# Optimization experiments

Measured on AMD Instinct MI355X. Metric: run time of the kernel, lower is better.

Reference implementation:

```python
import jax, jax.numpy as jnp
import numpy as np

B, S, D = 4, 4096, 1024


def setup_inputs() -> dict:
    key = jax.random.key(0)
    ks = jax.random.split(key, 7)
    scale = 1.0 / np.sqrt(D)
    return {
        "x": jax.random.normal(ks[0], (B, S, D), dtype=jnp.float32),
        "W_in": jax.random.normal(ks[1], (D, D), dtype=jnp.float32) * scale,
        "W_select": jax.random.normal(ks[2], (D, D), dtype=jnp.float32) * scale,
        "W_gate": jax.random.normal(ks[3], (D, D), dtype=jnp.float32) * scale,
        "W_out": jax.random.normal(ks[4], (D, D), dtype=jnp.float32) * scale,
        "W_delta": jax.random.normal(ks[5], (D, D), dtype=jnp.float32) * scale,
        "log_a": jax.random.normal(ks[6], (D,), dtype=jnp.float32) * 0.1,
    }


def reference(x, W_in, W_select, W_gate, W_out, W_delta, log_a):
    # diag mode of ChaosSSMCore. nn.Linear(bias=False): y = x @ W.T
    a_base = jax.nn.sigmoid(log_a).astype(x.dtype)  # [D]
    # Precompute all per-step projections in batched GEMMs: [B,S,D]
    delta = jnp.maximum(jax.nn.softplus(jnp.einsum('bsd,ed->bse', x, W_delta)), 1e-4)
    decay = jnp.exp(-delta * a_base)                                   # [B,S,D]
    update = jax.nn.sigmoid(jnp.einsum('bsd,ed->bse', x, W_select)) \
        * jnp.tanh(jnp.einsum('bsd,ed->bse', x, W_in))                 # [B,S,D]
    gate = jax.nn.sigmoid(jnp.einsum('bsd,ed->bse', x, W_gate))        # [B,S,D]

    def step(state, inputs):
        dec_t, upd_t = inputs
        state = dec_t * state + upd_t
        return state, state

    init = jnp.zeros((x.shape[0], x.shape[2]), dtype=x.dtype)
    # scan over seq axis: move to [S,B,D]
    _, states = jax.lax.scan(step, init, (decay.transpose(1, 0, 2), update.transpose(1, 0, 2)))
    states = states.transpose(1, 0, 2)  # [B,S,D]
    out = gate * states
    y = jnp.einsum('bsd,ed->bse', out, W_out)
    return y
```

## Files before the change

### kernel.cpp

```cpp
#include <hip/hip_runtime.h>
#include <hip/hip_bf16.h>
#include <math.h>

#define B_   4
#define S_   4096
#define D_   1024
#define M_   (B_*S_)
#define NCAT (4*D_)
#define KD   1024

#define NCHUNK 128
#define CHLEN  (S_/NCHUNK)

typedef __bf16 bf16x8 __attribute__((ext_vector_type(8)));
typedef float  f32x4  __attribute__((ext_vector_type(4)));
typedef ushort ushort8v __attribute__((ext_vector_type(8)));

__device__ __forceinline__ ushort sbf(float f) {
  return __builtin_bit_cast(ushort, (__bf16)f);
}
__device__ __forceinline__ uint pk2bf(float lo, float hi) {
  return (uint)sbf(lo) | ((uint)sbf(hi) << 16);
}
__device__ __forceinline__ float bf2f(uint bits16) {
  union { uint u; float f; } v; v.u = bits16 << 16;
  return v.f;
}

#define GLL(g, l) __builtin_amdgcn_global_load_lds( \
  (const __attribute__((address_space(1))) uint32_t*)(uintptr_t)(g), \
  (__attribute__((address_space(3))) uint32_t*)(uint32_t)(uintptr_t)(l), 16, 0, 0)

#define MFMA_(a, b, c) __builtin_amdgcn_mfma_f32_16x16x32_bf16(a, b, c, 0, 0, 0)

__global__ void k_cvt_f2b4(const float* __restrict__ in, ushort* __restrict__ out, int n4) {
  int i = blockIdx.x * blockDim.x + threadIdx.x;
  if (i >= n4) return;
  const float4 v = ((const float4*)in)[i];
  uint2 o;
  o.x = pk2bf(v.x, v.y);
  o.y = pk2bf(v.z, v.w);
  ((uint2*)out)[i] = o;
}

__global__ void k_build_wcat(const float* __restrict__ wdel, const float* __restrict__ wsel,
                             const float* __restrict__ win,  const float* __restrict__ wgat,
                             ushort* __restrict__ wcat) {
  int i = blockIdx.x * blockDim.x + threadIdx.x;
  int E = i * 4;
  int n   = E >> 10;
  int col = E & 1023;
  int p = (n >> 4) & 3;
  int e = ((n >> 6) << 4) + (n & 15);
  const float* src = (p == 0) ? wdel : (p == 1) ? wsel : (p == 2) ? win : wgat;
  const float4 v = *(const float4*)&src[(size_t)e * 1024 + col];
  uint2 o;
  o.x = pk2bf(v.x, v.y);
  o.y = pk2bf(v.z, v.w);
  *(uint2*)&wcat[E] = o;
}

__global__ void k_abase(const float* __restrict__ log_a, float* __restrict__ abase) {
  int i = blockIdx.x * blockDim.x + threadIdx.x;
  if (i < D_) abase[i] = 1.f / (1.f + __expf(-log_a[i]));
}

template<int MODE>
__global__ __launch_bounds__(512, 2) void gemm10(
    const ushort* __restrict__ Ab, const ushort* __restrict__ Bb, int nbn,
    float* __restrict__ outf,
    ushort* __restrict__ dec, ushort* __restrict__ uu, ushort* __restrict__ gat,
    const float* __restrict__ abase)
{
  __shared__ ushort lds[65536];

  const int nwg = gridDim.x;
  const int bid = blockIdx.x;
  const int nb  = (bid & 7) * (nwg >> 3) + (bid >> 3);
  const int brow = nb / nbn, bcol = nb % nbn;
  const int t = threadIdx.x, lane = t & 63, w = t >> 6;
  const int wm = w >> 2, wn = w & 3;
  const int l15 = lane & 15, lhi = lane >> 4;

  const int lr = t >> 2, cs = t & 3;
  const int csw = cs ^ ((lr >> 1) & 3);
  const int gA0 = (lr & 63) | ((lr & 64) << 1);
  const int gA1 = gA0 | 64;
  const int gB0 = (lr & 31) | ((lr & 0x60) << 1);
  const int gB1 = gB0 | 32;
  const uint vA0 = ((uint)(brow * 256 + gA0) * KD + (uint)csw * 8) * 2u;
  const uint vA1 = ((uint)(brow * 256 + gA1) * KD + (uint)csw * 8) * 2u;
  const uint vB0 = ((uint)(bcol * 256 + gB0) * KD + (uint)csw * 8) * 2u;
  const uint vB1 = ((uint)(bcol * 256 + gB1) * KD + (uint)csw * 8) * 2u;
  const char* Ab8 = (const char*)Ab;
  const char* Bb8 = (const char*)Bb;
  const int dstT = t * 8;

#define STG(PB, OPOFF, SRC8, VOFF, R, KO) do { \
    GLL((SRC8) + (VOFF) + (KO) * 2,      &lds[(PB) + (OPOFF) + (R) * 4096 + dstT]); \
    GLL((SRC8) + (VOFF) + (KO) * 2 + 64, &lds[(PB) + (OPOFF) + 8192 + (R) * 4096 + dstT]); } while (0)

  const int swp = (lhi ^ ((l15 >> 1) & 3)) * 8;
  const ushort* fA  = &lds[(wm * 64 + l15) * 32 + swp];
  const ushort* fB  = &lds[16384 + (wn * 32 + l15) * 32 + swp];

#define RD_A4(DST, PB, HOFF, KK) \
    _Pragma("unroll") for (int m = 0; m < 4; ++m) \
      DST[m][KK] = *(const bf16x8*)&fA[(PB) + (KK) * 8192 + (HOFF) + m * 512];
#define RD_B4(DST, PB, HOFF) \
    _Pragma("unroll") for (int n = 0; n < 2; ++n) \
    _Pragma("unroll") for (int kk = 0; kk < 2; ++kk) \
      DST[n][kk] = *(const bf16x8*)&fB[(PB) + kk * 8192 + (HOFF) + n * 512];
#define MM4(AR, BV, M0, N0) \
    _Pragma("unroll") for (int kk = 0; kk < 2; ++kk) \
    _Pragma("unroll") for (int m = 0; m < 4; ++m) \
    _Pragma("unroll") for (int n = 0; n < 2; ++n) \
      acc[(M0) + m][(N0) + n] = MFMA_(AR[m][kk], BV[n][kk], acc[(M0) + m][(N0) + n]);
#define BAR   __builtin_amdgcn_s_barrier()
#define PRIO1 __builtin_amdgcn_s_setprio(1)
#define PRIO0 __builtin_amdgcn_s_setprio(0)

  f32x4 acc[8][4] = {};
  bf16x8 a03[4][2], a47[4][2], b23[2][2], b01a[2][2], b01b[2][2];

#define KTILE(P, Q, KO, BU, BN) do { \
    RD_A4(a03, P, 0, 1) \
    RD_B4(b23, P, 4096) \
    PRIO1; MM4(a03, BU, 0, 0) PRIO0; BAR; \
    RD_A4(a47, P, 4096, 0) \
    STG(P, 16384, Bb8, vB0, 0, KO); \
    PRIO1; MM4(a03, b23, 0, 2) PRIO0; BAR; \
    RD_A4(a47, P, 4096, 1) \
    STG(P, 0, Ab8, vA0, 0, KO); \
    STG(P, 16384, Bb8, vB1, 1, KO); \
    PRIO1; MM4(a47, b23, 4, 2) PRIO0; \
    asm volatile("s_waitcnt vmcnt(6)" ::: "memory"); \
    BAR; \
    RD_A4(a03, Q, 0, 0) \
    RD_B4(BN, Q, 0) \
    STG(P, 0, Ab8, vA1, 1, KO); \
    PRIO1; MM4(a47, BU, 4, 0) PRIO0; BAR; \
  } while (0)

  STG(0, 16384, Bb8, vB0, 0, 0);
  STG(0, 0, Ab8, vA0, 0, 0);
  STG(0, 16384, Bb8, vB1, 1, 0);
  STG(0, 0, Ab8, vA1, 1, 0);
  STG(32768, 16384, Bb8, vB0, 0, 64);
  STG(32768, 0, Ab8, vA0, 0, 64);
  STG(32768, 16384, Bb8, vB1, 1, 64);
  STG(32768, 0, Ab8, vA1, 1, 64);
  asm volatile("s_waitcnt vmcnt(8)" ::: "memory");
  BAR;
  RD_A4(a03, 0, 0, 0)
  RD_B4(b01a, 0, 0)

#pragma unroll 1
  for (int i = 0; i < 8; ++i) {
    const int t2 = 2 * i + 2, t3 = 2 * i + 3;
    const int ko2 = (t2 < 16 ? t2 : 15) * 64;
    const int ko3 = (t3 < 16 ? t3 : 15) * 64;
    KTILE(0, 32768, ko2, b01a, b01b);
    KTILE(32768, 0, ko3, b01b, b01a);
  }

  asm volatile("s_waitcnt vmcnt(0)" ::: "memory");
  __syncthreads();

  const int rowb = wm * 128;
  if constexpr (MODE == 0) {
    ushort* ldsD = lds;
    ushort* ldsU = lds + 16384;
    ushort* ldsG = lds + 32768;
    const int chl = wn * 16 + l15;
    const int chg = bcol * 64 + chl;
    const float ab = abase[chg];
#pragma unroll
    for (int mf = 0; mf < 8; ++mf) {
      const int rl0 = rowb + mf * 16 + lhi * 4;
#pragma unroll
      for (int r = 0; r < 4; ++r) {
        const float zd = acc[mf][0][r];
        const float zs = acc[mf][1][r];
        const float zi = acc[mf][2][r];
        const float zg = acc[mf][3][r];
        float sp = fmaxf(zd, 0.f) + log1pf(__expf(-fabsf(zd)));
        sp = fmaxf(sp, 1e-4f);
        const float dv = __expf(-sp * ab);
        const float sv = 1.f / (1.f + __expf(-zs));
        float tt = __expf(-2.f * fabsf(zi));
        float tv = (1.f - tt) / (1.f + tt);
        tv = (zi < 0.f) ? -tv : tv;
        const float gv = 1.f / (1.f + __expf(-zg));
        const int row = rl0 + r;
        const int idx = row * 64 + ((((chl >> 3) ^ (row & 7)) << 3) | (chl & 7));
        ldsD[idx] = sbf(dv);
        ldsU[idx] = sbf(sv * tv);
        ldsG[idx] = sbf(gv);
      }
    }
    __syncthreads();
    const int srow = t >> 3, cD = t & 7;
    const size_t gbase = (size_t)(brow * 256) * D_ + bcol * 64 + cD * 8;
#pragma unroll
    for (int itp = 0; itp < 4; ++itp) {
      const int row = itp * 64 + srow;
      const int lidx = row * 64 + ((cD ^ (row & 7)) << 3);
      const size_t g = gbase + (size_t)row * D_;
      *(ushort8v*)&dec[g] = *(const ushort8v*)&ldsD[lidx];
      *(ushort8v*)&uu[g]  = *(const ushort8v*)&ldsU[lidx];
      *(ushort8v*)&gat[g] = *(const ushort8v*)&ldsG[lidx];
    }
  } else {
    const int colb = bcol * 256 + wn * 64;
#pragma unroll
    for (int mf = 0; mf < 8; ++mf) {
      const int rl0 = brow * 256 + rowb + mf * 16 + lhi * 4;
#pragma unroll
      for (int nf = 0; nf < 4; ++nf) {
        const int gc = colb + nf * 16 + l15;
#pragma unroll
        for (int r = 0; r < 4; ++r)
          outf[(size_t)(rl0 + r) * 1024 + gc] = acc[mf][nf][r];
      }
    }
  }
#undef KTILE
#undef STG
#undef RD_A4
#undef RD_B4
#undef MM4
}

__global__ __launch_bounds__(512) void k_scanA(
    const ushort* __restrict__ dec, const ushort* __restrict__ uu,
    float* __restrict__ cP, float* __restrict__ cL)
{
  const int t  = threadIdx.x;
  const int c  = blockIdx.x & (NCHUNK - 1);
  const int b  = blockIdx.x >> 7;
  const int e2 = t * 2;
  size_t base = ((size_t)b * S_ + (size_t)c * CHLEN) * D_ + e2;
  float P0 = 1.f, P1 = 1.f, L0 = 0.f, L1 = 0.f;
  for (int i = 0; i < CHLEN; ++i) {
    const uint dv = *(const uint*)(dec + base);
    const uint uv = *(const uint*)(uu + base);
    float d0 = bf2f(dv & 0xffffu), d1 = bf2f(dv >> 16);
    P0 *= d0; L0 = fmaf(d0, L0, bf2f(uv & 0xffffu));
    P1 *= d1; L1 = fmaf(d1, L1, bf2f(uv >> 16));
    base += D_;
  }
  size_t o = ((size_t)b * NCHUNK + c) * D_ + e2;
  cP[o] = P0; cP[o + 1] = P1; cL[o] = L0; cL[o + 1] = L1;
}

__global__ __launch_bounds__(64) void k_scanB(
    const float* __restrict__ cP, const float* __restrict__ cL, float* __restrict__ carry)
{
  const int idx = blockIdx.x * 64 + threadIdx.x;
  const int b = idx >> 10, e = idx & 1023;
  float st = 0.f;
  size_t base = (size_t)b * NCHUNK * D_ + e;
  for (int c = 0; c < NCHUNK; ++c) {
    size_t o = base + (size_t)c * D_;
    carry[o] = st;
    st = fmaf(cP[o], st, cL[o]);
  }
}

__global__ __launch_bounds__(512) void k_scanC(
    const ushort* __restrict__ dec, const ushort* __restrict__ uu,
    const ushort* __restrict__ gat, const float* __restrict__ carry,
    ushort* __restrict__ outb)
{
  const int t  = threadIdx.x;
  const int c  = blockIdx.x & (NCHUNK - 1);
  const int b  = blockIdx.x >> 7;
  const int e2 = t * 2;
  size_t co = ((size_t)b * NCHUNK + c) * D_ + e2;
  float s0 = carry[co], s1 = carry[co + 1];
  size_t base = ((size_t)b * S_ + (size_t)c * CHLEN) * D_ + e2;
  for (int i = 0; i < CHLEN; ++i) {
    const uint dv = *(const uint*)(dec + base);
    const uint uv = *(const uint*)(uu + base);
    const uint gv = *(const uint*)(gat + base);
    s0 = fmaf(bf2f(dv & 0xffffu), s0, bf2f(uv & 0xffffu));
    s1 = fmaf(bf2f(dv >> 16),     s1, bf2f(uv >> 16));
    float o0 = bf2f(gv & 0xffffu) * s0;
    float o1 = bf2f(gv >> 16)     * s1;
    *(uint*)(outb + base) = pk2bf(o0, o1);
    base += D_;
  }
}

extern "C" void kernel_launch(void* const* d_in, const int* in_sizes, int n_in,
                              void* d_out, int out_size, void* d_ws, size_t ws_size,
                              hipStream_t stream) {
  const float* x     = (const float*)d_in[0];
  const float* W_in  = (const float*)d_in[1];
  const float* W_sel = (const float*)d_in[2];
  const float* W_gat = (const float*)d_in[3];
  const float* W_out = (const float*)d_in[4];
  const float* W_del = (const float*)d_in[5];
  const float* log_a = (const float*)d_in[6];
  float* y = (float*)d_out;

  char* ws = (char*)d_ws;
  size_t off = 0;
  auto alloc = [&](size_t bytes) { char* p = ws + off; off += (bytes + 255) & ~(size_t)255; return p; };
  ushort* xbf   = (ushort*)alloc((size_t)M_ * D_ * 2);
  ushort* wcat  = (ushort*)alloc((size_t)NCAT * D_ * 2);
  ushort* woutb = (ushort*)alloc((size_t)D_ * D_ * 2);
  ushort* dec   = (ushort*)alloc((size_t)M_ * D_ * 2);
  ushort* uu    = (ushort*)alloc((size_t)M_ * D_ * 2);
  ushort* gat   = (ushort*)alloc((size_t)M_ * D_ * 2);
  float*  cP    = (float*)alloc((size_t)B_ * NCHUNK * D_ * 4);
  float*  cL    = (float*)alloc((size_t)B_ * NCHUNK * D_ * 4);
  float*  carry = (float*)alloc((size_t)B_ * NCHUNK * D_ * 4);
  float*  abase = (float*)alloc(D_ * 4);
  ushort* outb  = xbf;

  k_cvt_f2b4<<<(M_ * D_ / 4 + 255) / 256, 256, 0, stream>>>(x, xbf, M_ * D_ / 4);
  k_build_wcat<<<(NCAT * D_ / 4 + 255) / 256, 256, 0, stream>>>(W_del, W_sel, W_in, W_gat, wcat);
  k_cvt_f2b4<<<(D_ * D_ / 4 + 255) / 256, 256, 0, stream>>>(W_out, woutb, D_ * D_ / 4);
  k_abase<<<(D_ + 255) / 256, 256, 0, stream>>>(log_a, abase);

  gemm10<0><<<(M_ / 256) * (NCAT / 256), 512, 0, stream>>>(
      xbf, wcat, NCAT / 256, nullptr, dec, uu, gat, abase);

  k_scanA<<<B_ * NCHUNK, 512, 0, stream>>>(dec, uu, cP, cL);
  k_scanB<<<(B_ * D_) / 64, 64, 0, stream>>>(cP, cL, carry);
  k_scanC<<<B_ * NCHUNK, 512, 0, stream>>>(dec, uu, gat, carry, outb);

  gemm10<1><<<(M_ / 256) * (D_ / 256), 512, 0, stream>>>(
      outb, woutb, D_ / 256, y, nullptr, nullptr, nullptr, nullptr);
}
```

Baseline: 313.1 us.

## Restructure GEMM k-tile schedule with explicit LDS waits and no cross-tile fragment prefetch

Rewrites the GEMM main loop so each k-tile loads all its own A/B fragments from LDS (no register prefetch of the next tile's fragments), inserting explicit lgkmcnt(0) waits plus sched barriers before each MFMA group and reordering the global-to-LDS stages. The aim is a simpler, more predictable interleave of LDS reads, async global loads and MFMAs that the compiler cannot reorder badly. It trades away the latency hiding from cross-tile prefetching and adds extra barriers and full LDS waits, which can expose LDS latency.

```diff
diff --git a/kernel.cpp b/kernel.cpp
--- a/kernel.cpp
+++ b/kernel.cpp
@@ -66,7 +66,7 @@
 }
 
 template<int MODE>
-__global__ __launch_bounds__(512, 2) void gemm10(
+__global__ __launch_bounds__(512, 2) void gemm11(
     const ushort* __restrict__ Ab, const ushort* __restrict__ Bb, int nbn,
     float* __restrict__ outf,
     ushort* __restrict__ dec, ushort* __restrict__ uu, ushort* __restrict__ gat,
@@ -104,9 +104,10 @@
   const ushort* fA  = &lds[(wm * 64 + l15) * 32 + swp];
   const ushort* fB  = &lds[16384 + (wn * 32 + l15) * 32 + swp];
 
-#define RD_A4(DST, PB, HOFF, KK) \
+#define RD_A8(DST, PB, HOFF) \
     _Pragma("unroll") for (int m = 0; m < 4; ++m) \
-      DST[m][KK] = *(const bf16x8*)&fA[(PB) + (KK) * 8192 + (HOFF) + m * 512];
+    _Pragma("unroll") for (int kk = 0; kk < 2; ++kk) \
+      DST[m][kk] = *(const bf16x8*)&fA[(PB) + kk * 8192 + (HOFF) + m * 512];
 #define RD_B4(DST, PB, HOFF) \
     _Pragma("unroll") for (int n = 0; n < 2; ++n) \
     _Pragma("unroll") for (int kk = 0; kk < 2; ++kk) \
@@ -119,49 +120,51 @@
 #define BAR   __builtin_amdgcn_s_barrier()
 #define PRIO1 __builtin_amdgcn_s_setprio(1)
 #define PRIO0 __builtin_amdgcn_s_setprio(0)
+#define LGKM0 do { asm volatile("s_waitcnt lgkmcnt(0)" ::: "memory"); \
+                   __builtin_amdgcn_sched_barrier(0); } while (0)
 
   f32x4 acc[8][4] = {};
-  bf16x8 a03[4][2], a47[4][2], b23[2][2], b01a[2][2], b01b[2][2];
-
-#define KTILE(P, Q, KO, BU, BN) do { \
-    RD_A4(a03, P, 0, 1) \
+
+#define KTILE(P, KO) do { \
+    bf16x8 a03[4][2], a47[4][2], b01[2][2], b23[2][2]; \
+     \
+    RD_A8(a03, P, 0) RD_B4(b01, P, 0) \
+    BAR; LGKM0; \
+    PRIO1; MM4(a03, b01, 0, 0) PRIO0; BAR; \
+     \
     RD_B4(b23, P, 4096) \
-    PRIO1; MM4(a03, BU, 0, 0) PRIO0; BAR; \
-    RD_A4(a47, P, 4096, 0) \
+    STG(P, 0, Ab8, vA0, 0, KO); \
+    BAR; LGKM0; \
+    PRIO1; MM4(a03, b23, 0, 2) PRIO0; BAR; \
+     \
+    RD_A8(a47, P, 4096) \
     STG(P, 16384, Bb8, vB0, 0, KO); \
-    PRIO1; MM4(a03, b23, 0, 2) PRIO0; BAR; \
-    RD_A4(a47, P, 4096, 1) \
-    STG(P, 0, Ab8, vA0, 0, KO); \
+    BAR; LGKM0; \
+    PRIO1; MM4(a47, b23, 4, 2) PRIO0; BAR; \
+     \
     STG(P, 16384, Bb8, vB1, 1, KO); \
-    PRIO1; MM4(a47, b23, 4, 2) PRIO0; \
+    STG(P, 0, Ab8, vA1, 1, KO); \
     asm volatile("s_waitcnt vmcnt(6)" ::: "memory"); \
     BAR; \
-    RD_A4(a03, Q, 0, 0) \
-    RD_B4(BN, Q, 0) \
-    STG(P, 0, Ab8, vA1, 1, KO); \
-    PRIO1; MM4(a47, BU, 4, 0) PRIO0; BAR; \
+    PRIO1; MM4(a47, b01, 4, 0) PRIO0; BAR; \
   } while (0)
 
+  STG(0, 0, Ab8, vA0, 0, 0);
   STG(0, 16384, Bb8, vB0, 0, 0);
-  STG(0, 0, Ab8, vA0, 0, 0);
   STG(0, 16384, Bb8, vB1, 1, 0);
   STG(0, 0, Ab8, vA1, 1, 0);
+  STG(32768, 0, Ab8, vA0, 0, 64);
   STG(32768, 16384, Bb8, vB0, 0, 64);
-  STG(32768, 0, Ab8, vA0, 0, 64);
   STG(32768, 16384, Bb8, vB1, 1, 64);
   STG(32768, 0, Ab8, vA1, 1, 64);
   asm volatile("s_waitcnt vmcnt(8)" ::: "memory");
   BAR;
-  RD_A4(a03, 0, 0, 0)
-  RD_B4(b01a, 0, 0)
 
 #pragma unroll 1
-  for (int i = 0; i < 8; ++i) {
-    const int t2 = 2 * i + 2, t3 = 2 * i + 3;
-    const int ko2 = (t2 < 16 ? t2 : 15) * 64;
-    const int ko3 = (t3 < 16 ? t3 : 15) * 64;
-    KTILE(0, 32768, ko2, b01a, b01b);
-    KTILE(32768, 0, ko3, b01b, b01a);
+  for (int i = 0; i < 16; ++i) {
+    const int tn = i + 2;
+    const int ko = (tn < 16 ? tn : 15) * 64;
+    if (i & 1) KTILE(32768, ko); else KTILE(0, ko);
   }
 
   asm volatile("s_waitcnt vmcnt(0)" ::: "memory");
@@ -227,7 +230,7 @@
   }
 #undef KTILE
 #undef STG
-#undef RD_A4
+#undef RD_A8
 #undef RD_B4
 #undef MM4
 }
@@ -325,13 +328,13 @@
   k_cvt_f2b4<<<(D_ * D_ / 4 + 255) / 256, 256, 0, stream>>>(W_out, woutb, D_ * D_ / 4);
   k_abase<<<(D_ + 255) / 256, 256, 0, stream>>>(log_a, abase);
 
-  gemm10<0><<<(M_ / 256) * (NCAT / 256), 512, 0, stream>>>(
+  gemm11<0><<<(M_ / 256) * (NCAT / 256), 512, 0, stream>>>(
       xbf, wcat, NCAT / 256, nullptr, dec, uu, gat, abase);
 
   k_scanA<<<B_ * NCHUNK, 512, 0, stream>>>(dec, uu, cP, cL);
   k_scanB<<<(B_ * D_) / 64, 64, 0, stream>>>(cP, cL, carry);
   k_scanC<<<B_ * NCHUNK, 512, 0, stream>>>(dec, uu, gat, carry, outb);
 
-  gemm10<1><<<(M_ / 256) * (D_ / 256), 512, 0, stream>>>(
+  gemm11<1><<<(M_ / 256) * (D_ / 256), 512, 0, stream>>>(
       outb, woutb, D_ / 256, y, nullptr, nullptr, nullptr, nullptr);
 }
```

New measurement: 781.9 us. 2.5x slower.

## Fuse chunk-scan reduction into projection GEMM epilogue and use fast reciprocals

Applied to the files above, without the earlier changes.

Removes the separate k_scanA kernel. The first GEMM's epilogue now computes each chunk's decay product and local scan (P, L) directly from the bf16-rounded decay and update values. It combines them across lanes with wavefront shuffles and writes cP/cL. This saves a full re-read of the dec and uu tensors and one kernel launch. It also replaces divisions and log1pf with hardware rcp and __logf approximations, which adds a little epilogue register pressure and slightly changes accuracy.

```diff
diff --git a/kernel.cpp b/kernel.cpp
--- a/kernel.cpp
+++ b/kernel.cpp
@@ -26,6 +26,7 @@
   union { uint u; float f; } v; v.u = bits16 << 16;
   return v.f;
 }
+__device__ __forceinline__ float frcp(float x) { return __builtin_amdgcn_rcpf(x); }
 
 #define GLL(g, l) __builtin_amdgcn_global_load_lds( \
   (const __attribute__((address_space(1))) uint32_t*)(uintptr_t)(g), \
@@ -62,7 +63,7 @@
 
 __global__ void k_abase(const float* __restrict__ log_a, float* __restrict__ abase) {
   int i = blockIdx.x * blockDim.x + threadIdx.x;
-  if (i < D_) abase[i] = 1.f / (1.f + __expf(-log_a[i]));
+  if (i < D_) abase[i] = frcp(1.f + __expf(-log_a[i]));
 }
 
 template<int MODE>
@@ -70,7 +71,8 @@
     const ushort* __restrict__ Ab, const ushort* __restrict__ Bb, int nbn,
     float* __restrict__ outf,
     ushort* __restrict__ dec, ushort* __restrict__ uu, ushort* __restrict__ gat,
-    const float* __restrict__ abase)
+    const float* __restrict__ abase,
+    float* __restrict__ cP, float* __restrict__ cL)
 {
   __shared__ ushort lds[65536];
 
@@ -175,28 +177,61 @@
     const int chl = wn * 16 + l15;
     const int chg = bcol * 64 + chl;
     const float ab = abase[chg];
+    float Prun[8], Lrun[8];
 #pragma unroll
     for (int mf = 0; mf < 8; ++mf) {
       const int rl0 = rowb + mf * 16 + lhi * 4;
+      float P = 1.f, L = 0.f;
 #pragma unroll
       for (int r = 0; r < 4; ++r) {
         const float zd = acc[mf][0][r];
         const float zs = acc[mf][1][r];
         const float zi = acc[mf][2][r];
         const float zg = acc[mf][3][r];
-        float sp = fmaxf(zd, 0.f) + log1pf(__expf(-fabsf(zd)));
+        float sp = fmaxf(zd, 0.f) + __logf(1.f + __expf(-fabsf(zd)));
         sp = fmaxf(sp, 1e-4f);
         const float dv = __expf(-sp * ab);
-        const float sv = 1.f / (1.f + __expf(-zs));
+        const float sv = frcp(1.f + __expf(-zs));
         float tt = __expf(-2.f * fabsf(zi));
-        float tv = (1.f - tt) / (1.f + tt);
+        float tv = (1.f - tt) * frcp(1.f + tt);
         tv = (zi < 0.f) ? -tv : tv;
-        const float gv = 1.f / (1.f + __expf(-zg));
+        const float gv = frcp(1.f + __expf(-zg));
+        const ushort dbits = sbf(dv);
+        const ushort ubits = sbf(sv * tv);
         const int row = rl0 + r;
         const int idx = row * 64 + ((((chl >> 3) ^ (row & 7)) << 3) | (chl & 7));
-        ldsD[idx] = sbf(dv);
-        ldsU[idx] = sbf(sv * tv);
+        ldsD[idx] = dbits;
+        ldsU[idx] = ubits;
         ldsG[idx] = sbf(gv);
+        const float dq = bf2f(dbits), uq = bf2f(ubits);
+        P *= dq;
+        L = fmaf(dq, L, uq);
+      }
+      Prun[mf] = P; Lrun[mf] = L;
+    }
+    const int bq = brow >> 4;
+    const int cbase = (brow & 15) * 8 + wm * 4;
+#pragma unroll
+    for (int j = 0; j < 4; ++j) {
+      float Pe = Prun[2 * j],     Le = Lrun[2 * j];
+      float Po = Prun[2 * j + 1], Lo = Lrun[2 * j + 1];
+      {
+        float Pn = __shfl_down(Pe, 16), Ln = __shfl_down(Le, 16);
+        Pe = Pe * Pn; Le = fmaf(Pn, Le, Ln);
+        float Pm = __shfl_down(Po, 16), Lm = __shfl_down(Lo, 16);
+        Po = Po * Pm; Lo = fmaf(Pm, Lo, Lm);
+      }
+      {
+        float Pn = __shfl_down(Pe, 32), Ln = __shfl_down(Le, 32);
+        Pe = Pe * Pn; Le = fmaf(Pn, Le, Ln);
+        float Pm = __shfl_down(Po, 32), Lm = __shfl_down(Lo, 32);
+        Po = Po * Pm; Lo = fmaf(Pm, Lo, Lm);
+      }
+      if (lhi == 0) {
+        const float Pc = Pe * Po;
+        const float Lc = fmaf(Po, Le, Lo);
+        const size_t o = ((size_t)(bq * NCHUNK + cbase + j)) * D_ + chg;
+        cP[o] = Pc; cL[o] = Lc;
       }
     }
     __syncthreads();
@@ -230,28 +265,6 @@
 #undef RD_A4
 #undef RD_B4
 #undef MM4
-}
-
-__global__ __launch_bounds__(512) void k_scanA(
-    const ushort* __restrict__ dec, const ushort* __restrict__ uu,
-    float* __restrict__ cP, float* __restrict__ cL)
-{
-  const int t  = threadIdx.x;
-  const int c  = blockIdx.x & (NCHUNK - 1);
-  const int b  = blockIdx.x >> 7;
-  const int e2 = t * 2;
-  size_t base = ((size_t)b * S_ + (size_t)c * CHLEN) * D_ + e2;
-  float P0 = 1.f, P1 = 1.f, L0 = 0.f, L1 = 0.f;
-  for (int i = 0; i < CHLEN; ++i) {
-    const uint dv = *(const uint*)(dec + base);
-    const uint uv = *(const uint*)(uu + base);
-    float d0 = bf2f(dv & 0xffffu), d1 = bf2f(dv >> 16);
-    P0 *= d0; L0 = fmaf(d0, L0, bf2f(uv & 0xffffu));
-    P1 *= d1; L1 = fmaf(d1, L1, bf2f(uv >> 16));
-    base += D_;
-  }
-  size_t o = ((size_t)b * NCHUNK + c) * D_ + e2;
-  cP[o] = P0; cP[o + 1] = P1; cL[o] = L0; cL[o + 1] = L1;
 }
 
 __global__ __launch_bounds__(64) void k_scanB(
@@ -326,12 +339,11 @@
   k_abase<<<(D_ + 255) / 256, 256, 0, stream>>>(log_a, abase);
 
   gemm10<0><<<(M_ / 256) * (NCAT / 256), 512, 0, stream>>>(
-      xbf, wcat, NCAT / 256, nullptr, dec, uu, gat, abase);
-
-  k_scanA<<<B_ * NCHUNK, 512, 0, stream>>>(dec, uu, cP, cL);
+      xbf, wcat, NCAT / 256, nullptr, dec, uu, gat, abase, cP, cL);
+
   k_scanB<<<(B_ * D_) / 64, 64, 0, stream>>>(cP, cL, carry);
   k_scanC<<<B_ * NCHUNK, 512, 0, stream>>>(dec, uu, gat, carry, outb);
 
   gemm10<1><<<(M_ / 256) * (D_ / 256), 512, 0, stream>>>(
-      outb, woutb, D_ / 256, y, nullptr, nullptr, nullptr, nullptr);
-}
+      outb, woutb, D_ / 256, y, nullptr, nullptr, nullptr, nullptr, nullptr, nullptr);
+}
```

Result: faster. 256.7 us (-18.0%).
